# Optimization experiments

Measured on AMD Instinct MI355X. Metric: run time of the kernel, lower is better.

The kernel has to match this reference:

```python
import jax, jax.numpy as jnp
import numpy as np

NUM_HEADS = 32
NUM_KV_HEADS = 8
HEAD_DIM = 128
PAGE_SIZE = 16
NUM_PAGES = 512
PAGES_PER_SEQ = 256  # 4096 cached tokens
Q_LEN = 1024
SCALE = 0.08838834764831845  # 1/sqrt(HEAD_DIM)


def setup_inputs() -> dict:
    key = jax.random.key(0)
    k1, k2, k3, k4, k5 = jax.random.split(key, 5)
    q = jax.random.normal(k1, (Q_LEN, NUM_HEADS * HEAD_DIM), dtype=jnp.float32)
    k = jax.random.normal(k2, (Q_LEN, NUM_KV_HEADS * HEAD_DIM), dtype=jnp.float32)
    v = jax.random.normal(k3, (Q_LEN, NUM_KV_HEADS * HEAD_DIM), dtype=jnp.float32)
    # paged KV cache: [num_pages, 2 (k/v), num_kv_heads, page_size, head_dim]
    kv_cache = jax.random.normal(
        k4, (NUM_PAGES, 2, NUM_KV_HEADS, PAGE_SIZE, HEAD_DIM), dtype=jnp.float32)
    block_table = jnp.sort(
        jax.random.randint(k5, (PAGES_PER_SEQ,), 0, NUM_PAGES, dtype=jnp.int32))
    return {"q": q, "k": k, "v": v, "kv_cache": kv_cache,
            "block_table": block_table}


def reference(q, k, v, kv_cache, block_table):
    # reshape flat projections into heads
    q = q.reshape(-1, NUM_HEADS, HEAD_DIM)          # [Tq, H, D]
    k = k.reshape(-1, NUM_KV_HEADS, HEAD_DIM)       # [Tq, Hkv, D]
    v = v.reshape(-1, NUM_KV_HEADS, HEAD_DIM)

    # gather paged KV cache into continuous tensors (all pages full)
    pages = kv_cache[block_table]                   # [P, 2, Hkv, ps, D]
    # per-page [Hkv, ps, D] -> [ps, Hkv, D], then concat along token dim
    past = jnp.transpose(pages, (1, 0, 3, 2, 4))    # [2, P, ps, Hkv, D]
    past = past.reshape(2, -1, NUM_KV_HEADS, HEAD_DIM)
    past_k, past_v = past[0], past[1]               # [Tpast, Hkv, D]

    k_full = jnp.concatenate([past_k, k], axis=0)   # [Tkv, Hkv, D]
    v_full = jnp.concatenate([past_v, v], axis=0)

    # GQA: repeat kv heads to match query heads
    heads_per_kv = NUM_HEADS // NUM_KV_HEADS
    k_full = jnp.repeat(k_full, heads_per_kv, axis=1)  # [Tkv, H, D]
    v_full = jnp.repeat(v_full, heads_per_kv, axis=1)

    qh = jnp.transpose(q, (1, 0, 2))                # [H, Tq, D]
    kh = jnp.transpose(k_full, (1, 0, 2))           # [H, Tkv, D]
    vh = jnp.transpose(v_full, (1, 0, 2))

    scores = jnp.einsum('hqd,hkd->hqk', qh, kh) * SCALE  # [H, Tq, Tkv]

    # prefill causal mask exactly as in the source: triu(ones(q_len, kv_len), 1)
    q_len, kv_len = qh.shape[1], kh.shape[1]
    causal = jnp.triu(jnp.ones((q_len, kv_len), dtype=bool), k=1)
    scores = jnp.where(causal[None, :, :], -jnp.inf, scores)

    attn = jax.nn.softmax(scores.astype(jnp.float32), axis=-1).astype(qh.dtype)
    out = jnp.einsum('hqk,hkd->hqd', attn, vh)      # [H, Tq, D]
    out = jnp.transpose(out, (1, 0, 2)).reshape(-1, NUM_HEADS * HEAD_DIM)
    return out
```

## Files before the change

kernel.cpp:

```cpp
#include <hip/hip_runtime.h>
#include <hip/hip_bf16.h>


#define Q_STRIDE 4096
#define SCALE 0.08838834764831845f
#define RESCALE_THR 8.0f
#define KSW_TILE 16384
#define VSW_OFF  (2 * 1024 * 1024)
#define ACC1_OFF (4 * 1024 * 1024)
#define ML0_OFF  (ACC1_OFF + 32768 * 256)
#define ML1_OFF  (ML0_OFF + 32768 * 8)

typedef short short8 __attribute__((ext_vector_type(8)));
typedef float f32x4 __attribute__((ext_vector_type(4)));
typedef unsigned short ushort_t;
typedef unsigned int uint_t;

__device__ __forceinline__ ushort_t f2bf(float f) {
    return __builtin_bit_cast(ushort_t, __float2bfloat16(f));
}
__device__ __forceinline__ uint_t pk2(float a, float b) {
    return (uint_t)f2bf(a) | ((uint_t)f2bf(b) << 16);
}
__device__ __forceinline__ float bf2f(ushort_t u) {
    uint_t x = ((uint_t)u) << 16;
    return __builtin_bit_cast(float, x);
}

__launch_bounds__(256)
__global__ void prep_kv(const float* __restrict__ kvc,
                        const int* __restrict__ bt,
                        char* __restrict__ wsb)
{
    __shared__ float sVt[64 * 128];
    const int blk = blockIdx.x;
    const int hkv = blk >> 4;
    const int jb  = blk & 15;
    const int tid = threadIdx.x;
    char* kout = wsb + (size_t)(hkv * 16 + jb) * KSW_TILE;
    char* vout = wsb + VSW_OFF + (size_t)(hkv * 16 + jb) * KSW_TILE;

#pragma unroll
    for (int i = 0; i < 4; ++i) {
        const int u = tid + i * 256;
        const int t = u >> 4, c = u & 15;
        const int gtok = jb * 64 + t;
        const int page = bt[gtok >> 4];
        const float* src = kvc + (size_t)page * 32768 + (size_t)hkv * 2048
                         + (gtok & 15) * 128 + c * 8;
        float4 a = *(const float4*)src;
        float4 b = *(const float4*)(src + 4);
        uint4 p;
        p.x = pk2(a.x, a.y); p.y = pk2(a.z, a.w);
        p.z = pk2(b.x, b.y); p.w = pk2(b.z, b.w);
        *(uint4*)(kout + t * 256 + ((c * 16) ^ ((t & 7) << 4))) = p;
    }
#pragma unroll
    for (int i = 0; i < 8; ++i) {
        const int u = tid + i * 256;
        const int t = u >> 5, c4 = u & 31;
        const int gtok = jb * 64 + t;
        const int page = bt[gtok >> 4];
        const float* src = kvc + (size_t)page * 32768 + 16384
                         + (size_t)hkv * 2048 + (gtok & 15) * 128 + c4 * 4;
        *(float4*)(sVt + t * 128 + c4 * 4) = *(const float4*)src;
    }
    __syncthreads();
#pragma unroll
    for (int i = 0; i < 4; ++i) {
        const int u = tid + i * 256;
        const int d = u >> 3, ch = u & 7;
        float v[8];
#pragma unroll
        for (int k = 0; k < 8; ++k) v[k] = sVt[(8 * ch + k) * 128 + d];
        uint4 p;
        p.x = pk2(v[0], v[1]); p.y = pk2(v[2], v[3]);
        p.z = pk2(v[4], v[5]); p.w = pk2(v[6], v[7]);
        *(uint4*)(vout + ((d * 128 + 16 * ch) ^ ((d & 7) << 4))) = p;
    }
}

#define GLL16(G, L) __builtin_amdgcn_global_load_lds(                         \
    (const uint_t __attribute__((address_space(1)))*)(G),                     \
    (uint_t __attribute__((address_space(3)))*)(L), 16, 0, 0)

#define STAGE(JB, KB, VB) {                                                   \
    const char* b_ = kvbf + (size_t)(hkv * 16 + (JB)) * KSW_TILE              \
                   + w * 1024 + lane * 16;                                    \
    GLL16(b_,                  (KB) + w * 1024);                              \
    GLL16(b_ + 8192,           (KB) + w * 1024 + 8192);                       \
    GLL16(b_ + VSW_OFF,        (VB) + w * 1024);                              \
    GLL16(b_ + VSW_OFF + 8192, (VB) + w * 1024 + 8192);                       \
}

__launch_bounds__(512)
__global__ void attn_main(const float* __restrict__ q,
                          const char* __restrict__ kvbf,
                          float* __restrict__ out,
                          char* __restrict__ wsb)
{
    __shared__ __align__(16) char sK[2][16384];
    __shared__ __align__(16) char sV[2][16384];
    __shared__ __align__(16) char sP[8][2048];

    const int bid  = blockIdx.x;
    const int half = bid >> 8;
    const int rr   = bid & 255;
    const int g    = rr >> 4;
    const int hp   = rr & 15;
    const int qt   = half ? g : (15 - g);
    const int nt   = qt + 1;
    const int nt0  = (nt + 1) >> 1;
    const int jb0  = half ? nt0 : 0;
    const int jb1  = half ? nt  : nt0;
    const int hkv  = hp >> 1;
    const int tid  = threadIdx.x;
    const int w    = tid >> 6;
    const int lane = tid & 63;
    const int l15  = lane & 15;
    const int lhi  = lane >> 4;
    const int h    = hp * 2 + (w >> 2);
    const int rg   = w & 3;

    short8 qf[4];
    {
        const int qrow = qt * 64 + rg * 16 + l15;
        const float* qp = q + (size_t)qrow * Q_STRIDE + h * 128;
#pragma unroll
        for (int s = 0; s < 4; ++s) {
            const int d0 = s * 32 + lhi * 8;
            float4 a = *(const float4*)(qp + d0);
            float4 b = *(const float4*)(qp + d0 + 4);
            short8 v;
            v[0] = (short)f2bf(a.x * SCALE); v[1] = (short)f2bf(a.y * SCALE);
            v[2] = (short)f2bf(a.z * SCALE); v[3] = (short)f2bf(a.w * SCALE);
            v[4] = (short)f2bf(b.x * SCALE); v[5] = (short)f2bf(b.y * SCALE);
            v[6] = (short)f2bf(b.z * SCALE); v[7] = (short)f2bf(b.w * SCALE);
            qf[s] = v;
        }
    }

    f32x4 acc[8];
#pragma unroll
    for (int n2 = 0; n2 < 8; ++n2) acc[n2] = (f32x4){0.f, 0.f, 0.f, 0.f};
    float m_run[4]  = {-1e30f, -1e30f, -1e30f, -1e30f};
    float l_part[4] = {0.f, 0.f, 0.f, 0.f};

    if (jb0 < jb1) {
        STAGE(jb0, sK[0], sV[0])
    }
    __syncthreads();

    for (int jb = jb0; jb < jb1; ++jb) {
        const int cur = (jb - jb0) & 1;
        char* kbuf = sK[cur];
        char* vbuf = sV[cur];
        const bool pf = (jb + 1 < jb1);
        if (pf) {
            STAGE(jb + 1, sK[cur ^ 1], sV[cur ^ 1])
        }

        f32x4 sacc[4];
#pragma unroll
        for (int n = 0; n < 4; ++n) sacc[n] = (f32x4){0.f, 0.f, 0.f, 0.f};
#pragma unroll
        for (int s = 0; s < 4; ++s) {
#pragma unroll
            for (int n = 0; n < 4; ++n) {
                const int tok = n * 16 + l15;
                const uint_t byte = (uint_t)(tok * 256)
                    + (((uint_t)((s * 32 + lhi * 8) * 2)) ^ ((uint_t)((tok & 7) << 4)));
                short8 kb = *(const short8*)(kbuf + byte);
                sacc[n] = __builtin_amdgcn_mfma_f32_16x16x32_bf16(qf[s], kb, sacc[n], 0, 0, 0);
            }
        }

        const bool diag = (jb == qt);
        if (diag) {
#pragma unroll
            for (int n = 0; n < 4; ++n)
#pragma unroll
                for (int j = 0; j < 4; ++j) {
                    const int tok = jb * 64 + n * 16 + l15;
                    const int qg  = qt * 64 + rg * 16 + lhi * 4 + j;
                    if (tok > qg) sacc[n][j] = -1e30f;
                }
        }
#pragma unroll
        for (int j = 0; j < 4; ++j) {
            float lmax = fmaxf(fmaxf(sacc[0][j], sacc[1][j]),
                               fmaxf(sacc[2][j], sacc[3][j]));
            if (__any(lmax > m_run[j] + RESCALE_THR)) {
                float mt = lmax;
#pragma unroll
                for (int off = 1; off < 16; off <<= 1)
                    mt = fmaxf(mt, __shfl_xor(mt, off));
                const float mn = fmaxf(m_run[j], mt);
                const float alpha = __expf(m_run[j] - mn);
                m_run[j] = mn;
                l_part[j] *= alpha;
#pragma unroll
                for (int n2 = 0; n2 < 8; ++n2) acc[n2][j] *= alpha;
            }
            float ls = 0.f;
#pragma unroll
            for (int n = 0; n < 4; ++n) {
                float p = __expf(sacc[n][j] - m_run[j]);
                sacc[n][j] = p;
                ls += p;
            }
            l_part[j] += ls;
        }

        char* pb = sP[w];
#pragma unroll
        for (int n = 0; n < 4; ++n)
#pragma unroll
            for (int j = 0; j < 4; ++j) {
                const int r = lhi * 4 + j;
                const uint_t byte = (uint_t)(r * 128)
                    + (((uint_t)((n * 16 + l15) * 2)) ^ ((uint_t)((r & 7) << 4)));
                *(ushort_t*)(pb + byte) = f2bf(sacc[n][j]);
            }

#pragma unroll
        for (int s2 = 0; s2 < 2; ++s2) {
            const uint_t pbyte = (uint_t)(l15 * 128)
                + (((uint_t)((s2 * 32 + lhi * 8) * 2)) ^ ((uint_t)((l15 & 7) << 4)));
            short8 pa = *(const short8*)(pb + pbyte);
#pragma unroll
            for (int n2 = 0; n2 < 8; ++n2) {
                const int dim = n2 * 16 + l15;
                const uint_t vbyte = (uint_t)(dim * 128)
                    + (((uint_t)((s2 * 32 + lhi * 8) * 2)) ^ ((uint_t)((dim & 7) << 4)));
                short8 vbf = *(const short8*)(vbuf + vbyte);
                acc[n2] = __builtin_amdgcn_mfma_f32_16x16x32_bf16(pa, vbf, acc[n2], 0, 0, 0);
            }
        }

        if (pf) __syncthreads();
    }

#pragma unroll
    for (int j = 0; j < 4; ++j) {
        float lsum = l_part[j];
#pragma unroll
        for (int off = 1; off < 16; off <<= 1)
            lsum += __shfl_xor(lsum, off);
        const int row64 = rg * 16 + lhi * 4 + j;
        const int qg    = qt * 64 + row64;
        const int idx   = (qt * 32 + h) * 64 + row64;
        if (half == 0) {
            float* dst = out + (size_t)qg * Q_STRIDE + h * 128;
#pragma unroll
            for (int n2 = 0; n2 < 8; ++n2)
                dst[n2 * 16 + l15] = acc[n2][j];
            if (l15 == 0) {
                float* ml = (float*)(wsb + ML0_OFF) + (size_t)idx * 2;
                ml[0] = m_run[j]; ml[1] = lsum;
            }
        } else {
            ushort_t* dst = (ushort_t*)(wsb + ACC1_OFF) + (size_t)idx * 128;
#pragma unroll
            for (int n2 = 0; n2 < 8; ++n2)
                dst[n2 * 16 + l15] = f2bf(acc[n2][j]);
            if (l15 == 0) {
                float* ml = (float*)(wsb + ML1_OFF) + (size_t)idx * 2;
                ml[0] = m_run[j]; ml[1] = lsum;
            }
        }
    }
}

__launch_bounds__(256)
__global__ void attn_combine(float* __restrict__ out, const char* __restrict__ wsb)
{
    const int pid = blockIdx.x;
    const int qt = pid >> 5;
    const int h  = pid & 31;
    const int tid = threadIdx.x;
    const int d4  = (tid & 31) * 4;
    const float* ml0b = (const float*)(wsb + ML0_OFF);
    const float* ml1b = (const float*)(wsb + ML1_OFF);
    const ushort_t* a1b = (const ushort_t*)(wsb + ACC1_OFF);

#pragma unroll
    for (int p = 0; p < 8; ++p) {
        const int r = (tid >> 5) + p * 8;
        const size_t idx = (size_t)pid * 64 + r;
        const float m1 = ml0b[idx * 2], l1 = ml0b[idx * 2 + 1];
        const float m2 = ml1b[idx * 2], l2 = ml1b[idx * 2 + 1];
        const float m  = fmaxf(m1, m2);
        const float a1 = __expf(m1 - m), a2 = __expf(m2 - m);
        const float inv = 1.0f / (l1 * a1 + l2 * a2);
        float* o = out + (size_t)(qt * 64 + r) * Q_STRIDE + h * 128 + d4;
        const ushort_t* y4 = a1b + idx * 128 + d4;
        float4 x = *(const float4*)o;
        x.x = (x.x * a1 + bf2f(y4[0]) * a2) * inv;
        x.y = (x.y * a1 + bf2f(y4[1]) * a2) * inv;
        x.z = (x.z * a1 + bf2f(y4[2]) * a2) * inv;
        x.w = (x.w * a1 + bf2f(y4[3]) * a2) * inv;
        *(float4*)o = x;
    }
}

extern "C" void kernel_launch(void* const* d_in, const int* in_sizes, int n_in,
                              void* d_out, int out_size, void* d_ws, size_t ws_size,
                              hipStream_t stream) {
    const float* q   = (const float*)d_in[0];
    const float* kvc = (const float*)d_in[3];
    const int*   bt  = (const int*)d_in[4];
    float* out = (float*)d_out;
    char*  wsb = (char*)d_ws;
    prep_kv<<<dim3(128), dim3(256), 0, stream>>>(kvc, bt, wsb);
    attn_main<<<dim3(512), dim3(512), 0, stream>>>(q, wsb, out, wsb);
    attn_combine<<<dim3(512), dim3(256), 0, stream>>>(out, wsb);
}
```

Baseline: 54.37 us.

## Split attention into per-head 32-token tiles with selective split-KV

```diff
diff --git a/kernel.cpp b/kernel.cpp
--- a/kernel.cpp
+++ b/kernel.cpp
@@ -8,8 +8,8 @@
 #define KSW_TILE 16384
 #define VSW_OFF  (2 * 1024 * 1024)
 #define ACC1_OFF (4 * 1024 * 1024)
-#define ML0_OFF  (ACC1_OFF + 32768 * 256)
-#define ML1_OFF  (ML0_OFF + 32768 * 8)
+#define ML0_OFF  (ACC1_OFF + 16384 * 256)
+#define ML1_OFF  (ML0_OFF + 16384 * 8)
 
 typedef short short8 __attribute__((ext_vector_type(8)));
 typedef float f32x4 __attribute__((ext_vector_type(4)));
@@ -70,13 +70,15 @@
     for (int i = 0; i < 4; ++i) {
         const int u = tid + i * 256;
         const int d = u >> 3, ch = u & 7;
+        const int half = ch >> 2, ch2 = ch & 3;
         float v[8];
 #pragma unroll
-        for (int k = 0; k < 8; ++k) v[k] = sVt[(8 * ch + k) * 128 + d];
+        for (int k = 0; k < 8; ++k)
+            v[k] = sVt[(half * 32 + ch2 * 8 + k) * 128 + d];
         uint4 p;
         p.x = pk2(v[0], v[1]); p.y = pk2(v[2], v[3]);
         p.z = pk2(v[4], v[5]); p.w = pk2(v[6], v[7]);
-        *(uint4*)(vout + ((d * 128 + 16 * ch) ^ ((d & 7) << 4))) = p;
+        *(uint4*)(vout + half * 8192 + d * 64 + ((ch2 * 16) ^ ((d & 3) << 4))) = p;
     }
 }
 
@@ -84,43 +86,50 @@
     (const uint_t __attribute__((address_space(1)))*)(G),                     \
     (uint_t __attribute__((address_space(3)))*)(L), 16, 0, 0)
 
-#define STAGE(JB, KB, VB) {                                                   \
-    const char* b_ = kvbf + (size_t)(hkv * 16 + (JB)) * KSW_TILE              \
-                   + w * 1024 + lane * 16;                                    \
-    GLL16(b_,                  (KB) + w * 1024);                              \
-    GLL16(b_ + 8192,           (KB) + w * 1024 + 8192);                       \
-    GLL16(b_ + VSW_OFF,        (VB) + w * 1024);                              \
-    GLL16(b_ + VSW_OFF + 8192, (VB) + w * 1024 + 8192);                       \
-}
-
-__launch_bounds__(512)
+#define STAGE(JB2, KB, VB) {                                                  \
+    const char* ks_ = kvbf + (size_t)hkv * 262144 + (size_t)(JB2) * 8192      \
+                    + w * 2048 + lane * 16;                                   \
+    GLL16(ks_,                  (KB) + w * 2048);                             \
+    GLL16(ks_ + 1024,           (KB) + w * 2048 + 1024);                      \
+    GLL16(ks_ + VSW_OFF,        (VB) + w * 2048);                             \
+    GLL16(ks_ + VSW_OFF + 1024, (VB) + w * 2048 + 1024);                      \
+}
+
+__launch_bounds__(256)
 __global__ void attn_main(const float* __restrict__ q,
                           const char* __restrict__ kvbf,
                           float* __restrict__ out,
                           char* __restrict__ wsb)
 {
-    __shared__ __align__(16) char sK[2][16384];
-    __shared__ __align__(16) char sV[2][16384];
-    __shared__ __align__(16) char sP[8][2048];
-
-    const int bid  = blockIdx.x;
-    const int half = bid >> 8;
-    const int rr   = bid & 255;
-    const int g    = rr >> 4;
-    const int hp   = rr & 15;
-    const int qt   = half ? g : (15 - g);
-    const int nt   = qt + 1;
-    const int nt0  = (nt + 1) >> 1;
-    const int jb0  = half ? nt0 : 0;
-    const int jb1  = half ? nt  : nt0;
-    const int hkv  = hp >> 1;
+    __shared__ __align__(16) char sK[2][8192];
+    __shared__ __align__(16) char sV[2][8192];
+    __shared__ __align__(16) char sP[4][1024];
+
+    const int bid = blockIdx.x;
+    int qt, jb0, jb1, mode, h;
+    if (bid < 512) {
+        const int half = bid & 1;
+        const int idx  = bid >> 1;
+        qt  = 15 - (idx >> 5);
+        h   = idx & 31;
+        const int nt = qt + 1;
+        jb0 = half ? nt : 0;
+        jb1 = half ? 2 * nt : nt;
+        mode = half ? 2 : 1;
+    } else {
+        const int idx2 = bid - 512;
+        qt  = 7 - (idx2 >> 5);
+        h   = idx2 & 31;
+        jb0 = 0; jb1 = 2 * (qt + 1);
+        mode = 0;
+    }
+    const int hkv = h >> 2;
     const int tid  = threadIdx.x;
     const int w    = tid >> 6;
     const int lane = tid & 63;
     const int l15  = lane & 15;
     const int lhi  = lane >> 4;
-    const int h    = hp * 2 + (w >> 2);
-    const int rg   = w & 3;
+    const int rg   = w;
 
     short8 qf[4];
     {
@@ -146,27 +155,26 @@
     float m_run[4]  = {-1e30f, -1e30f, -1e30f, -1e30f};
     float l_part[4] = {0.f, 0.f, 0.f, 0.f};
 
-    if (jb0 < jb1) {
-        STAGE(jb0, sK[0], sV[0])
-    }
+    STAGE(jb0, sK[0], sV[0])
     __syncthreads();
 
-    for (int jb = jb0; jb < jb1; ++jb) {
-        const int cur = (jb - jb0) & 1;
+    char* pb = sP[w];
+    for (int jb2 = jb0; jb2 < jb1; ++jb2) {
+        const int cur = (jb2 - jb0) & 1;
         char* kbuf = sK[cur];
         char* vbuf = sV[cur];
-        const bool pf = (jb + 1 < jb1);
+        const bool pf = (jb2 + 1 < jb1);
         if (pf) {
-            STAGE(jb + 1, sK[cur ^ 1], sV[cur ^ 1])
-        }
-
-        f32x4 sacc[4];
-#pragma unroll
-        for (int n = 0; n < 4; ++n) sacc[n] = (f32x4){0.f, 0.f, 0.f, 0.f};
+            STAGE(jb2 + 1, sK[cur ^ 1], sV[cur ^ 1])
+        }
+
+        f32x4 sacc[2];
+#pragma unroll
+        for (int n = 0; n < 2; ++n) sacc[n] = (f32x4){0.f, 0.f, 0.f, 0.f};
 #pragma unroll
         for (int s = 0; s < 4; ++s) {
 #pragma unroll
-            for (int n = 0; n < 4; ++n) {
+            for (int n = 0; n < 2; ++n) {
                 const int tok = n * 16 + l15;
                 const uint_t byte = (uint_t)(tok * 256)
                     + (((uint_t)((s * 32 + lhi * 8) * 2)) ^ ((uint_t)((tok & 7) << 4)));
@@ -175,21 +183,19 @@
             }
         }
 
-        const bool diag = (jb == qt);
-        if (diag) {
-#pragma unroll
-            for (int n = 0; n < 4; ++n)
+        if (jb2 >= 2 * qt) {
+#pragma unroll
+            for (int n = 0; n < 2; ++n)
 #pragma unroll
                 for (int j = 0; j < 4; ++j) {
-                    const int tok = jb * 64 + n * 16 + l15;
+                    const int tok = jb2 * 32 + n * 16 + l15;
                     const int qg  = qt * 64 + rg * 16 + lhi * 4 + j;
                     if (tok > qg) sacc[n][j] = -1e30f;
                 }
         }
 #pragma unroll
         for (int j = 0; j < 4; ++j) {
-            float lmax = fmaxf(fmaxf(sacc[0][j], sacc[1][j]),
-                               fmaxf(sacc[2][j], sacc[3][j]));
+            float lmax = fmaxf(sacc[0][j], sacc[1][j]);
             if (__any(lmax > m_run[j] + RESCALE_THR)) {
                 float mt = lmax;
 #pragma unroll
@@ -204,7 +210,7 @@
             }
             float ls = 0.f;
 #pragma unroll
-            for (int n = 0; n < 4; ++n) {
+            for (int n = 0; n < 2; ++n) {
                 float p = __expf(sacc[n][j] - m_run[j]);
                 sacc[n][j] = p;
                 ls += p;
@@ -212,27 +218,25 @@
             l_part[j] += ls;
         }
 
-        char* pb = sP[w];
-#pragma unroll
-        for (int n = 0; n < 4; ++n)
+#pragma unroll
+        for (int n = 0; n < 2; ++n)
 #pragma unroll
             for (int j = 0; j < 4; ++j) {
                 const int r = lhi * 4 + j;
-                const uint_t byte = (uint_t)(r * 128)
-                    + (((uint_t)((n * 16 + l15) * 2)) ^ ((uint_t)((r & 7) << 4)));
+                const uint_t byte = (uint_t)(r * 64)
+                    + (((uint_t)((n * 16 + l15) * 2)) ^ ((uint_t)((r & 3) << 4)));
                 *(ushort_t*)(pb + byte) = f2bf(sacc[n][j]);
             }
 
-#pragma unroll
-        for (int s2 = 0; s2 < 2; ++s2) {
-            const uint_t pbyte = (uint_t)(l15 * 128)
-                + (((uint_t)((s2 * 32 + lhi * 8) * 2)) ^ ((uint_t)((l15 & 7) << 4)));
+        {
+            const uint_t pbyte = (uint_t)(l15 * 64)
+                + (((uint_t)(lhi * 16)) ^ ((uint_t)((l15 & 3) << 4)));
             short8 pa = *(const short8*)(pb + pbyte);
 #pragma unroll
             for (int n2 = 0; n2 < 8; ++n2) {
                 const int dim = n2 * 16 + l15;
-                const uint_t vbyte = (uint_t)(dim * 128)
-                    + (((uint_t)((s2 * 32 + lhi * 8) * 2)) ^ ((uint_t)((dim & 7) << 4)));
+                const uint_t vbyte = (uint_t)(dim * 64)
+                    + (((uint_t)(lhi * 16)) ^ ((uint_t)((dim & 3) << 4)));
                 short8 vbf = *(const short8*)(vbuf + vbyte);
                 acc[n2] = __builtin_amdgcn_mfma_f32_16x16x32_bf16(pa, vbf, acc[n2], 0, 0, 0);
             }
@@ -249,24 +253,32 @@
             lsum += __shfl_xor(lsum, off);
         const int row64 = rg * 16 + lhi * 4 + j;
         const int qg    = qt * 64 + row64;
-        const int idx   = (qt * 32 + h) * 64 + row64;
-        if (half == 0) {
+        if (mode == 0) {
+            const float inv = 1.0f / lsum;
             float* dst = out + (size_t)qg * Q_STRIDE + h * 128;
 #pragma unroll
             for (int n2 = 0; n2 < 8; ++n2)
-                dst[n2 * 16 + l15] = acc[n2][j];
-            if (l15 == 0) {
-                float* ml = (float*)(wsb + ML0_OFF) + (size_t)idx * 2;
-                ml[0] = m_run[j]; ml[1] = lsum;
-            }
+                dst[n2 * 16 + l15] = acc[n2][j] * inv;
         } else {
-            ushort_t* dst = (ushort_t*)(wsb + ACC1_OFF) + (size_t)idx * 128;
-#pragma unroll
-            for (int n2 = 0; n2 < 8; ++n2)
-                dst[n2 * 16 + l15] = f2bf(acc[n2][j]);
-            if (l15 == 0) {
-                float* ml = (float*)(wsb + ML1_OFF) + (size_t)idx * 2;
-                ml[0] = m_run[j]; ml[1] = lsum;
+            const int idx = ((qt - 8) * 32 + h) * 64 + row64;
+            if (mode == 1) {
+                float* dst = out + (size_t)qg * Q_STRIDE + h * 128;
+#pragma unroll
+                for (int n2 = 0; n2 < 8; ++n2)
+                    dst[n2 * 16 + l15] = acc[n2][j];
+                if (l15 == 0) {
+                    float* ml = (float*)(wsb + ML0_OFF) + (size_t)idx * 2;
+                    ml[0] = m_run[j]; ml[1] = lsum;
+                }
+            } else {
+                ushort_t* dst = (ushort_t*)(wsb + ACC1_OFF) + (size_t)idx * 128;
+#pragma unroll
+                for (int n2 = 0; n2 < 8; ++n2)
+                    dst[n2 * 16 + l15] = f2bf(acc[n2][j]);
+                if (l15 == 0) {
+                    float* ml = (float*)(wsb + ML1_OFF) + (size_t)idx * 2;
+                    ml[0] = m_run[j]; ml[1] = lsum;
+                }
             }
         }
     }
@@ -276,7 +288,7 @@
 __global__ void attn_combine(float* __restrict__ out, const char* __restrict__ wsb)
 {
     const int pid = blockIdx.x;
-    const int qt = pid >> 5;
+    const int qt = 8 + (pid >> 5);
     const int h  = pid & 31;
     const int tid = threadIdx.x;
     const int d4  = (tid & 31) * 4;
@@ -313,6 +325,6 @@
     float* out = (float*)d_out;
     char*  wsb = (char*)d_ws;
     prep_kv<<<dim3(128), dim3(256), 0, stream>>>(kvc, bt, wsb);
-    attn_main<<<dim3(512), dim3(512), 0, stream>>>(q, wsb, out, wsb);
-    attn_combine<<<dim3(512), dim3(256), 0, stream>>>(out, wsb);
-}
+    attn_main<<<dim3(768), dim3(256), 0, stream>>>(q, wsb, out, wsb);
+    attn_combine<<<dim3(256), dim3(256), 0, stream>>>(out, wsb);
+}
```

Result: slower. 58.57 us (+7.7%).

## Switch attention to 32x32x16 MFMA with register-resident P and GQA-grouped blocks

Applied to the files above, without the earlier changes.

```diff
diff --git a/kernel.cpp b/kernel.cpp
--- a/kernel.cpp
+++ b/kernel.cpp
@@ -12,9 +12,10 @@
 #define ML1_OFF  (ML0_OFF + 32768 * 8)
 
 typedef short short8 __attribute__((ext_vector_type(8)));
-typedef float f32x4 __attribute__((ext_vector_type(4)));
+typedef float f32x16 __attribute__((ext_vector_type(16)));
+typedef unsigned int uint_t;
+typedef uint_t u32x4 __attribute__((ext_vector_type(4)));
 typedef unsigned short ushort_t;
-typedef unsigned int uint_t;
 
 __device__ __forceinline__ ushort_t f2bf(float f) {
     return __builtin_bit_cast(ushort_t, __float2bfloat16(f));
@@ -53,7 +54,7 @@
         uint4 p;
         p.x = pk2(a.x, a.y); p.y = pk2(a.z, a.w);
         p.z = pk2(b.x, b.y); p.w = pk2(b.z, b.w);
-        *(uint4*)(kout + t * 256 + ((c * 16) ^ ((t & 7) << 4))) = p;
+        *(uint4*)(kout + t * 256 + ((c ^ (t & 15)) << 4)) = p;
     }
 #pragma unroll
     for (int i = 0; i < 8; ++i) {
@@ -76,7 +77,7 @@
         uint4 p;
         p.x = pk2(v[0], v[1]); p.y = pk2(v[2], v[3]);
         p.z = pk2(v[4], v[5]); p.w = pk2(v[6], v[7]);
-        *(uint4*)(vout + ((d * 128 + 16 * ch) ^ ((d & 7) << 4))) = p;
+        *(uint4*)(vout + d * 128 + ((ch ^ (d & 7)) << 4)) = p;
     }
 }
 
@@ -86,14 +87,18 @@
 
 #define STAGE(JB, KB, VB) {                                                   \
     const char* b_ = kvbf + (size_t)(hkv * 16 + (JB)) * KSW_TILE              \
-                   + w * 1024 + lane * 16;                                    \
-    GLL16(b_,                  (KB) + w * 1024);                              \
-    GLL16(b_ + 8192,           (KB) + w * 1024 + 8192);                       \
-    GLL16(b_ + VSW_OFF,        (VB) + w * 1024);                              \
-    GLL16(b_ + VSW_OFF + 8192, (VB) + w * 1024 + 8192);                       \
-}
-
-__launch_bounds__(512)
+                   + w * 4096 + lane * 16;                                    \
+    GLL16(b_,                  (KB) + w * 4096);                              \
+    GLL16(b_ + 1024,           (KB) + w * 4096 + 1024);                       \
+    GLL16(b_ + 2048,           (KB) + w * 4096 + 2048);                       \
+    GLL16(b_ + 3072,           (KB) + w * 4096 + 3072);                       \
+    GLL16(b_ + VSW_OFF,        (VB) + w * 4096);                              \
+    GLL16(b_ + VSW_OFF + 1024, (VB) + w * 4096 + 1024);                       \
+    GLL16(b_ + VSW_OFF + 2048, (VB) + w * 4096 + 2048);                       \
+    GLL16(b_ + VSW_OFF + 3072, (VB) + w * 4096 + 3072);                       \
+}
+
+__launch_bounds__(256)
 __global__ void attn_main(const float* __restrict__ q,
                           const char* __restrict__ kvbf,
                           float* __restrict__ out,
@@ -101,34 +106,30 @@
 {
     __shared__ __align__(16) char sK[2][16384];
     __shared__ __align__(16) char sV[2][16384];
-    __shared__ __align__(16) char sP[8][2048];
 
     const int bid  = blockIdx.x;
     const int half = bid >> 8;
-    const int rr   = bid & 255;
-    const int g    = rr >> 4;
-    const int hp   = rr & 15;
-    const int qt   = half ? g : (15 - g);
-    const int nt   = qt + 1;
+    const int r8   = bid & 255;
+    const int hkv  = r8 >> 5;
+    const int rt   = r8 & 31;
+    const int nt   = (rt >> 1) + 1;
     const int nt0  = (nt + 1) >> 1;
     const int jb0  = half ? nt0 : 0;
-    const int jb1  = half ? nt  : nt0;
-    const int hkv  = hp >> 1;
+    const int jb1  = half ? nt : nt0;
     const int tid  = threadIdx.x;
     const int w    = tid >> 6;
     const int lane = tid & 63;
-    const int l15  = lane & 15;
-    const int lhi  = lane >> 4;
-    const int h    = hp * 2 + (w >> 2);
-    const int rg   = w & 3;
-
-    short8 qf[4];
+    const int l31  = lane & 31;
+    const int hi   = lane >> 5;
+    const int hi4  = hi * 4;
+    const int h    = hkv * 4 + w;
+
+    short8 qf[8];
     {
-        const int qrow = qt * 64 + rg * 16 + l15;
-        const float* qp = q + (size_t)qrow * Q_STRIDE + h * 128;
-#pragma unroll
-        for (int s = 0; s < 4; ++s) {
-            const int d0 = s * 32 + lhi * 8;
+        const float* qp = q + (size_t)(rt * 32 + l31) * Q_STRIDE + h * 128;
+#pragma unroll
+        for (int ks = 0; ks < 8; ++ks) {
+            const int d0 = ks * 16 + hi * 8;
             float4 a = *(const float4*)(qp + d0);
             float4 b = *(const float4*)(qp + d0 + 4);
             short8 v;
@@ -136,15 +137,17 @@
             v[2] = (short)f2bf(a.z * SCALE); v[3] = (short)f2bf(a.w * SCALE);
             v[4] = (short)f2bf(b.x * SCALE); v[5] = (short)f2bf(b.y * SCALE);
             v[6] = (short)f2bf(b.z * SCALE); v[7] = (short)f2bf(b.w * SCALE);
-            qf[s] = v;
-        }
-    }
-
-    f32x4 acc[8];
-#pragma unroll
-    for (int n2 = 0; n2 < 8; ++n2) acc[n2] = (f32x4){0.f, 0.f, 0.f, 0.f};
-    float m_run[4]  = {-1e30f, -1e30f, -1e30f, -1e30f};
-    float l_part[4] = {0.f, 0.f, 0.f, 0.f};
+            qf[ks] = v;
+        }
+    }
+
+    f32x16 acc[4];
+#pragma unroll
+    for (int db = 0; db < 4; ++db)
+#pragma unroll
+        for (int r = 0; r < 16; ++r) acc[db][r] = 0.f;
+    float m_run  = -1e30f;
+    float l_part = 0.f;
 
     if (jb0 < jb1) {
         STAGE(jb0, sK[0], sV[0])
@@ -153,121 +156,135 @@
 
     for (int jb = jb0; jb < jb1; ++jb) {
         const int cur = (jb - jb0) & 1;
-        char* kbuf = sK[cur];
-        char* vbuf = sV[cur];
+        const char* kbuf = sK[cur];
+        const char* vbuf = sV[cur];
         const bool pf = (jb + 1 < jb1);
         if (pf) {
             STAGE(jb + 1, sK[cur ^ 1], sV[cur ^ 1])
         }
 
-        f32x4 sacc[4];
-#pragma unroll
-        for (int n = 0; n < 4; ++n) sacc[n] = (f32x4){0.f, 0.f, 0.f, 0.f};
-#pragma unroll
-        for (int s = 0; s < 4; ++s) {
-#pragma unroll
-            for (int n = 0; n < 4; ++n) {
-                const int tok = n * 16 + l15;
-                const uint_t byte = (uint_t)(tok * 256)
-                    + (((uint_t)((s * 32 + lhi * 8) * 2)) ^ ((uint_t)((tok & 7) << 4)));
-                short8 kb = *(const short8*)(kbuf + byte);
-                sacc[n] = __builtin_amdgcn_mfma_f32_16x16x32_bf16(qf[s], kb, sacc[n], 0, 0, 0);
-            }
-        }
-
-        const bool diag = (jb == qt);
+        f32x16 s0, s1;
+#pragma unroll
+        for (int r = 0; r < 16; ++r) { s0[r] = 0.f; s1[r] = 0.f; }
+        __builtin_amdgcn_s_setprio(1);
+#pragma unroll
+        for (int ks = 0; ks < 8; ++ks) {
+            const uint_t c0 = (uint_t)(((ks * 2 + hi) ^ (l31 & 15)) << 4);
+            short8 ka0 = *(const short8*)(kbuf + l31 * 256 + c0);
+            short8 ka1 = *(const short8*)(kbuf + 8192 + l31 * 256 + c0);
+            s0 = __builtin_amdgcn_mfma_f32_32x32x16_bf16(ka0, qf[ks], s0, 0, 0, 0);
+            s1 = __builtin_amdgcn_mfma_f32_32x32x16_bf16(ka1, qf[ks], s1, 0, 0, 0);
+        }
+        __builtin_amdgcn_s_setprio(0);
+
+        const bool diag = (jb == nt - 1);
         if (diag) {
-#pragma unroll
-            for (int n = 0; n < 4; ++n)
-#pragma unroll
-                for (int j = 0; j < 4; ++j) {
-                    const int tok = jb * 64 + n * 16 + l15;
-                    const int qg  = qt * 64 + rg * 16 + lhi * 4 + j;
-                    if (tok > qg) sacc[n][j] = -1e30f;
+            if (rt & 1) {
+#pragma unroll
+                for (int r = 0; r < 16; ++r) {
+                    const int treg = (r & 3) + 8 * (r >> 2) + hi4;
+                    if (treg > l31) s1[r] = -1e30f;
                 }
-        }
-#pragma unroll
-        for (int j = 0; j < 4; ++j) {
-            float lmax = fmaxf(fmaxf(sacc[0][j], sacc[1][j]),
-                               fmaxf(sacc[2][j], sacc[3][j]));
-            if (__any(lmax > m_run[j] + RESCALE_THR)) {
-                float mt = lmax;
-#pragma unroll
-                for (int off = 1; off < 16; off <<= 1)
-                    mt = fmaxf(mt, __shfl_xor(mt, off));
-                const float mn = fmaxf(m_run[j], mt);
-                const float alpha = __expf(m_run[j] - mn);
-                m_run[j] = mn;
-                l_part[j] *= alpha;
-#pragma unroll
-                for (int n2 = 0; n2 < 8; ++n2) acc[n2][j] *= alpha;
-            }
-            float ls = 0.f;
-#pragma unroll
-            for (int n = 0; n < 4; ++n) {
-                float p = __expf(sacc[n][j] - m_run[j]);
-                sacc[n][j] = p;
-                ls += p;
-            }
-            l_part[j] += ls;
-        }
-
-        char* pb = sP[w];
-#pragma unroll
-        for (int n = 0; n < 4; ++n)
-#pragma unroll
-            for (int j = 0; j < 4; ++j) {
-                const int r = lhi * 4 + j;
-                const uint_t byte = (uint_t)(r * 128)
-                    + (((uint_t)((n * 16 + l15) * 2)) ^ ((uint_t)((r & 7) << 4)));
-                *(ushort_t*)(pb + byte) = f2bf(sacc[n][j]);
-            }
-
-#pragma unroll
-        for (int s2 = 0; s2 < 2; ++s2) {
-            const uint_t pbyte = (uint_t)(l15 * 128)
-                + (((uint_t)((s2 * 32 + lhi * 8) * 2)) ^ ((uint_t)((l15 & 7) << 4)));
-            short8 pa = *(const short8*)(pb + pbyte);
-#pragma unroll
-            for (int n2 = 0; n2 < 8; ++n2) {
-                const int dim = n2 * 16 + l15;
-                const uint_t vbyte = (uint_t)(dim * 128)
-                    + (((uint_t)((s2 * 32 + lhi * 8) * 2)) ^ ((uint_t)((dim & 7) << 4)));
-                short8 vbf = *(const short8*)(vbuf + vbyte);
-                acc[n2] = __builtin_amdgcn_mfma_f32_16x16x32_bf16(pa, vbf, acc[n2], 0, 0, 0);
-            }
-        }
+            } else {
+#pragma unroll
+                for (int r = 0; r < 16; ++r) {
+                    const int treg = (r & 3) + 8 * (r >> 2) + hi4;
+                    if (treg > l31) s0[r] = -1e30f;
+                    s1[r] = -1e30f;
+                }
+            }
+        }
+
+        float pm = s0[0];
+#pragma unroll
+        for (int r = 1; r < 16; ++r) pm = fmaxf(pm, s0[r]);
+#pragma unroll
+        for (int r = 0; r < 16; ++r) pm = fmaxf(pm, s1[r]);
+        const float rmax = fmaxf(pm, __shfl_xor(pm, 32));
+        if (__any(rmax > m_run + RESCALE_THR)) {
+            const float mn = fmaxf(m_run, rmax);
+            const float al = __expf(m_run - mn);
+            m_run = mn;
+            l_part *= al;
+#pragma unroll
+            for (int r = 0; r < 16; ++r) {
+                const float ar = __shfl(al, (r & 3) + 8 * (r >> 2) + hi4);
+#pragma unroll
+                for (int db = 0; db < 4; ++db) acc[db][r] *= ar;
+            }
+        }
+        float ls = 0.f;
+#pragma unroll
+        for (int r = 0; r < 16; ++r) {
+            float e0 = __expf(s0[r] - m_run);
+            float e1 = __expf(s1[r] - m_run);
+            s0[r] = e0; s1[r] = e1;
+            ls += e0 + e1;
+        }
+        l_part += ls;
+
+        short8 pa[4];
+#pragma unroll
+        for (int hf = 0; hf < 2; ++hf) {
+            const f32x16& s = hf ? s1 : s0;
+            uint_t w0 = pk2(s[0],  s[1]),  w1 = pk2(s[2],  s[3]);
+            uint_t w2 = pk2(s[4],  s[5]),  w3 = pk2(s[6],  s[7]);
+            uint_t w4 = pk2(s[8],  s[9]),  w5 = pk2(s[10], s[11]);
+            uint_t w6 = pk2(s[12], s[13]), w7 = pk2(s[14], s[15]);
+            const uint_t sA = __shfl_xor(hi ? w0 : w2, 32);
+            const uint_t sB = __shfl_xor(hi ? w1 : w3, 32);
+            const uint_t sC = __shfl_xor(hi ? w4 : w6, 32);
+            const uint_t sD = __shfl_xor(hi ? w5 : w7, 32);
+            u32x4 f0, f1;
+            f0[0] = hi ? sA : w0; f0[1] = hi ? sB : w1;
+            f0[2] = hi ? w2 : sA; f0[3] = hi ? w3 : sB;
+            f1[0] = hi ? sC : w4; f1[1] = hi ? sD : w5;
+            f1[2] = hi ? w6 : sC; f1[3] = hi ? w7 : sD;
+            pa[hf * 2]     = __builtin_bit_cast(short8, f0);
+            pa[hf * 2 + 1] = __builtin_bit_cast(short8, f1);
+        }
+
+        __builtin_amdgcn_s_setprio(1);
+#pragma unroll
+        for (int kf = 0; kf < 4; ++kf) {
+#pragma unroll
+            for (int db = 0; db < 4; ++db) {
+                const uint_t byte = (uint_t)(db * 4096 + l31 * 128)
+                    + (uint_t)((((kf << 1) + hi) ^ (l31 & 7)) << 4);
+                short8 vb = *(const short8*)(vbuf + byte);
+                acc[db] = __builtin_amdgcn_mfma_f32_32x32x16_bf16(pa[kf], vb, acc[db], 0, 0, 0);
+            }
+        }
+        __builtin_amdgcn_s_setprio(0);
 
         if (pf) __syncthreads();
     }
 
-#pragma unroll
-    for (int j = 0; j < 4; ++j) {
-        float lsum = l_part[j];
-#pragma unroll
-        for (int off = 1; off < 16; off <<= 1)
-            lsum += __shfl_xor(lsum, off);
-        const int row64 = rg * 16 + lhi * 4 + j;
-        const int qg    = qt * 64 + row64;
-        const int idx   = (qt * 32 + h) * 64 + row64;
-        if (half == 0) {
-            float* dst = out + (size_t)qg * Q_STRIDE + h * 128;
-#pragma unroll
-            for (int n2 = 0; n2 < 8; ++n2)
-                dst[n2 * 16 + l15] = acc[n2][j];
-            if (l15 == 0) {
-                float* ml = (float*)(wsb + ML0_OFF) + (size_t)idx * 2;
-                ml[0] = m_run[j]; ml[1] = lsum;
-            }
-        } else {
-            ushort_t* dst = (ushort_t*)(wsb + ACC1_OFF) + (size_t)idx * 128;
-#pragma unroll
-            for (int n2 = 0; n2 < 8; ++n2)
-                dst[n2 * 16 + l15] = f2bf(acc[n2][j]);
-            if (l15 == 0) {
-                float* ml = (float*)(wsb + ML1_OFF) + (size_t)idx * 2;
-                ml[0] = m_run[j]; ml[1] = lsum;
-            }
+    const float l_row = l_part + __shfl_xor(l_part, 32);
+    if (half == 0) {
+#pragma unroll
+        for (int db = 0; db < 4; ++db)
+#pragma unroll
+            for (int r = 0; r < 16; ++r) {
+                const int qg = rt * 32 + (r & 3) + 8 * (r >> 2) + hi4;
+                out[(size_t)qg * Q_STRIDE + h * 128 + db * 32 + l31] = acc[db][r];
+            }
+        if (lane < 32) {
+            float* ml = (float*)(wsb + ML0_OFF) + (size_t)(h * 1024 + rt * 32 + l31) * 2;
+            ml[0] = m_run; ml[1] = l_row;
+        }
+    } else {
+        ushort_t* a1b = (ushort_t*)(wsb + ACC1_OFF);
+#pragma unroll
+        for (int db = 0; db < 4; ++db)
+#pragma unroll
+            for (int r = 0; r < 16; ++r) {
+                const int qg = rt * 32 + (r & 3) + 8 * (r >> 2) + hi4;
+                a1b[(size_t)(h * 1024 + qg) * 128 + db * 32 + l31] = f2bf(acc[db][r]);
+            }
+        if (lane < 32) {
+            float* ml = (float*)(wsb + ML1_OFF) + (size_t)(h * 1024 + rt * 32 + l31) * 2;
+            ml[0] = m_run; ml[1] = l_row;
         }
     }
 }
@@ -276,8 +293,8 @@
 __global__ void attn_combine(float* __restrict__ out, const char* __restrict__ wsb)
 {
     const int pid = blockIdx.x;
-    const int qt = pid >> 5;
-    const int h  = pid & 31;
+    const int h   = pid >> 4;
+    const int qb  = (pid & 15) * 64;
     const int tid = threadIdx.x;
     const int d4  = (tid & 31) * 4;
     const float* ml0b = (const float*)(wsb + ML0_OFF);
@@ -287,13 +304,13 @@
 #pragma unroll
     for (int p = 0; p < 8; ++p) {
         const int r = (tid >> 5) + p * 8;
-        const size_t idx = (size_t)pid * 64 + r;
+        const size_t idx = (size_t)h * 1024 + qb + r;
         const float m1 = ml0b[idx * 2], l1 = ml0b[idx * 2 + 1];
         const float m2 = ml1b[idx * 2], l2 = ml1b[idx * 2 + 1];
         const float m  = fmaxf(m1, m2);
         const float a1 = __expf(m1 - m), a2 = __expf(m2 - m);
         const float inv = 1.0f / (l1 * a1 + l2 * a2);
-        float* o = out + (size_t)(qt * 64 + r) * Q_STRIDE + h * 128 + d4;
+        float* o = out + (size_t)(qb + r) * Q_STRIDE + h * 128 + d4;
         const ushort_t* y4 = a1b + idx * 128 + d4;
         float4 x = *(const float4*)o;
         x.x = (x.x * a1 + bf2f(y4[0]) * a2) * inv;
@@ -313,6 +330,6 @@
     float* out = (float*)d_out;
     char*  wsb = (char*)d_ws;
     prep_kv<<<dim3(128), dim3(256), 0, stream>>>(kvc, bt, wsb);
-    attn_main<<<dim3(512), dim3(512), 0, stream>>>(q, wsb, out, wsb);
+    attn_main<<<dim3(512), dim3(256), 0, stream>>>(q, wsb, out, wsb);
     attn_combine<<<dim3(512), dim3(256), 0, stream>>>(out, wsb);
 }
```

Result: slower. 61.20 us (+12.6%).

## Restructure attention work split: two heads per wave, split only long q-tiles

Applied to the files above, without the earlier changes.

```diff
diff --git a/kernel.cpp b/kernel.cpp
--- a/kernel.cpp
+++ b/kernel.cpp
@@ -8,8 +8,8 @@
 #define KSW_TILE 16384
 #define VSW_OFF  (2 * 1024 * 1024)
 #define ACC1_OFF (4 * 1024 * 1024)
-#define ML0_OFF  (ACC1_OFF + 32768 * 256)
-#define ML1_OFF  (ML0_OFF + 32768 * 8)
+#define ML0_OFF  (ACC1_OFF + 16384 * 256)
+#define ML1_OFF  (ML0_OFF + 16384 * 8)
 
 typedef short short8 __attribute__((ext_vector_type(8)));
 typedef float f32x4 __attribute__((ext_vector_type(4)));
@@ -85,15 +85,64 @@
     (uint_t __attribute__((address_space(3)))*)(L), 16, 0, 0)
 
 #define STAGE(JB, KB, VB) {                                                   \
-    const char* b_ = kvbf + (size_t)(hkv * 16 + (JB)) * KSW_TILE              \
-                   + w * 1024 + lane * 16;                                    \
-    GLL16(b_,                  (KB) + w * 1024);                              \
-    GLL16(b_ + 8192,           (KB) + w * 1024 + 8192);                       \
-    GLL16(b_ + VSW_OFF,        (VB) + w * 1024);                              \
-    GLL16(b_ + VSW_OFF + 8192, (VB) + w * 1024 + 8192);                       \
-}
-
-__launch_bounds__(512)
+    const char* ks = kvbf + (size_t)(hkv * 16 + (JB)) * KSW_TILE              \
+                   + w * 4096 + lane * 16;                                    \
+    const char* vs = ks + VSW_OFF;                                            \
+    _Pragma("unroll")                                                         \
+    for (int i = 0; i < 4; ++i) {                                             \
+        GLL16(ks + i * 1024, (KB) + w * 4096 + i * 1024);                     \
+        GLL16(vs + i * 1024, (VB) + w * 4096 + i * 1024);                     \
+    }                                                                         \
+}
+
+#define SOFTMAX_P(SACC, MRUN, LPART, ACC, PB) {                               \
+    if (diag) {                                                               \
+        _Pragma("unroll")                                                     \
+        for (int n = 0; n < 4; ++n)                                           \
+            _Pragma("unroll")                                                 \
+            for (int j = 0; j < 4; ++j) {                                     \
+                const int tok = jb * 64 + n * 16 + l15;                       \
+                const int qg  = qt * 64 + rg * 16 + lhi * 4 + j;              \
+                if (tok > qg) SACC[n][j] = -1e30f;                            \
+            }                                                                 \
+    }                                                                         \
+    _Pragma("unroll")                                                         \
+    for (int j = 0; j < 4; ++j) {                                             \
+        float lmax = fmaxf(fmaxf(SACC[0][j], SACC[1][j]),                     \
+                           fmaxf(SACC[2][j], SACC[3][j]));                    \
+        if (__any(lmax > MRUN[j] + RESCALE_THR)) {                            \
+            float mt = lmax;                                                  \
+            _Pragma("unroll")                                                 \
+            for (int off = 1; off < 16; off <<= 1)                            \
+                mt = fmaxf(mt, __shfl_xor(mt, off));                          \
+            const float mn = fmaxf(MRUN[j], mt);                              \
+            const float alpha = __expf(MRUN[j] - mn);                         \
+            MRUN[j] = mn;                                                     \
+            LPART[j] *= alpha;                                                \
+            _Pragma("unroll")                                                 \
+            for (int n2 = 0; n2 < 8; ++n2) ACC[n2][j] *= alpha;               \
+        }                                                                     \
+        float ls = 0.f;                                                       \
+        _Pragma("unroll")                                                     \
+        for (int n = 0; n < 4; ++n) {                                         \
+            float p = __expf(SACC[n][j] - MRUN[j]);                           \
+            SACC[n][j] = p;                                                   \
+            ls += p;                                                          \
+        }                                                                     \
+        LPART[j] += ls;                                                       \
+    }                                                                         \
+    _Pragma("unroll")                                                         \
+    for (int n = 0; n < 4; ++n)                                               \
+        _Pragma("unroll")                                                     \
+        for (int j = 0; j < 4; ++j) {                                         \
+            const int r = lhi * 4 + j;                                        \
+            const uint_t byte = (uint_t)(r * 128)                             \
+                + (((uint_t)((n * 16 + l15) * 2)) ^ ((uint_t)((r & 7) << 4)));\
+            *(ushort_t*)((PB) + byte) = f2bf(SACC[n][j]);                     \
+        }                                                                     \
+}
+
+__launch_bounds__(256)
 __global__ void attn_main(const float* __restrict__ q,
                           const char* __restrict__ kvbf,
                           float* __restrict__ out,
@@ -101,31 +150,44 @@
 {
     __shared__ __align__(16) char sK[2][16384];
     __shared__ __align__(16) char sV[2][16384];
-    __shared__ __align__(16) char sP[8][2048];
-
-    const int bid  = blockIdx.x;
-    const int half = bid >> 8;
-    const int rr   = bid & 255;
-    const int g    = rr >> 4;
-    const int hp   = rr & 15;
-    const int qt   = half ? g : (15 - g);
-    const int nt   = qt + 1;
-    const int nt0  = (nt + 1) >> 1;
-    const int jb0  = half ? nt0 : 0;
-    const int jb1  = half ? nt  : nt0;
-    const int hkv  = hp >> 1;
+    __shared__ __align__(16) char sP[4][2][2048];
+
+    const int bid = blockIdx.x;
+    int qt, jb0, jb1, h0, hkv, mode;
+    bool two;
+    if (bid < 256) {
+        const int half = bid & 1;
+        const int idx  = bid >> 1;
+        qt  = 15 - (idx >> 4);
+        const int hp = idx & 15;
+        h0  = hp * 2;
+        hkv = hp >> 1;
+        const int nt  = qt + 1;
+        const int nt0 = (nt + 1) >> 1;
+        jb0 = half ? nt0 : 0;
+        jb1 = half ? nt : nt0;
+        mode = half ? 2 : 1;
+        two = true;
+    } else {
+        const int didx = bid - 256;
+        qt  = 7 - (didx >> 5);
+        h0  = didx & 31;
+        hkv = h0 >> 2;
+        jb0 = 0; jb1 = qt + 1;
+        mode = 0;
+        two = false;
+    }
     const int tid  = threadIdx.x;
     const int w    = tid >> 6;
     const int lane = tid & 63;
     const int l15  = lane & 15;
     const int lhi  = lane >> 4;
-    const int h    = hp * 2 + (w >> 2);
-    const int rg   = w & 3;
-
-    short8 qf[4];
+    const int rg   = w;
+
+    short8 qfA[4], qfB[4];
     {
         const int qrow = qt * 64 + rg * 16 + l15;
-        const float* qp = q + (size_t)qrow * Q_STRIDE + h * 128;
+        const float* qp = q + (size_t)qrow * Q_STRIDE + h0 * 128;
 #pragma unroll
         for (int s = 0; s < 4; ++s) {
             const int d0 = s * 32 + lhi * 8;
@@ -136,19 +198,32 @@
             v[2] = (short)f2bf(a.z * SCALE); v[3] = (short)f2bf(a.w * SCALE);
             v[4] = (short)f2bf(b.x * SCALE); v[5] = (short)f2bf(b.y * SCALE);
             v[6] = (short)f2bf(b.z * SCALE); v[7] = (short)f2bf(b.w * SCALE);
-            qf[s] = v;
-        }
-    }
-
-    f32x4 acc[8];
-#pragma unroll
-    for (int n2 = 0; n2 < 8; ++n2) acc[n2] = (f32x4){0.f, 0.f, 0.f, 0.f};
-    float m_run[4]  = {-1e30f, -1e30f, -1e30f, -1e30f};
-    float l_part[4] = {0.f, 0.f, 0.f, 0.f};
-
-    if (jb0 < jb1) {
-        STAGE(jb0, sK[0], sV[0])
-    }
+            qfA[s] = v;
+            if (two) {
+                float4 a2 = *(const float4*)(qp + 128 + d0);
+                float4 b2 = *(const float4*)(qp + 128 + d0 + 4);
+                short8 v2;
+                v2[0] = (short)f2bf(a2.x * SCALE); v2[1] = (short)f2bf(a2.y * SCALE);
+                v2[2] = (short)f2bf(a2.z * SCALE); v2[3] = (short)f2bf(a2.w * SCALE);
+                v2[4] = (short)f2bf(b2.x * SCALE); v2[5] = (short)f2bf(b2.y * SCALE);
+                v2[6] = (short)f2bf(b2.z * SCALE); v2[7] = (short)f2bf(b2.w * SCALE);
+                qfB[s] = v2;
+            }
+        }
+    }
+
+    f32x4 accA[8], accB[8];
+#pragma unroll
+    for (int n2 = 0; n2 < 8; ++n2) {
+        accA[n2] = (f32x4){0.f, 0.f, 0.f, 0.f};
+        accB[n2] = (f32x4){0.f, 0.f, 0.f, 0.f};
+    }
+    float mA[4] = {-1e30f, -1e30f, -1e30f, -1e30f};
+    float lA[4] = {0.f, 0.f, 0.f, 0.f};
+    float mB[4] = {-1e30f, -1e30f, -1e30f, -1e30f};
+    float lB[4] = {0.f, 0.f, 0.f, 0.f};
+
+    STAGE(jb0, sK[0], sV[0])
     __syncthreads();
 
     for (int jb = jb0; jb < jb1; ++jb) {
@@ -158,11 +233,20 @@
         const bool pf = (jb + 1 < jb1);
         if (pf) {
             STAGE(jb + 1, sK[cur ^ 1], sV[cur ^ 1])
-        }
-
-        f32x4 sacc[4];
-#pragma unroll
-        for (int n = 0; n < 4; ++n) sacc[n] = (f32x4){0.f, 0.f, 0.f, 0.f};
+            asm volatile("s_waitcnt vmcnt(8)" ::: "memory");
+        } else {
+            asm volatile("s_waitcnt vmcnt(0)" ::: "memory");
+        }
+        __builtin_amdgcn_sched_barrier(0);
+        __builtin_amdgcn_s_barrier();
+        __builtin_amdgcn_sched_barrier(0);
+
+        f32x4 saccA[4], saccB[4];
+#pragma unroll
+        for (int n = 0; n < 4; ++n) {
+            saccA[n] = (f32x4){0.f, 0.f, 0.f, 0.f};
+            saccB[n] = (f32x4){0.f, 0.f, 0.f, 0.f};
+        }
 #pragma unroll
         for (int s = 0; s < 4; ++s) {
 #pragma unroll
@@ -171,102 +255,89 @@
                 const uint_t byte = (uint_t)(tok * 256)
                     + (((uint_t)((s * 32 + lhi * 8) * 2)) ^ ((uint_t)((tok & 7) << 4)));
                 short8 kb = *(const short8*)(kbuf + byte);
-                sacc[n] = __builtin_amdgcn_mfma_f32_16x16x32_bf16(qf[s], kb, sacc[n], 0, 0, 0);
+                saccA[n] = __builtin_amdgcn_mfma_f32_16x16x32_bf16(qfA[s], kb, saccA[n], 0, 0, 0);
+                if (two)
+                    saccB[n] = __builtin_amdgcn_mfma_f32_16x16x32_bf16(qfB[s], kb, saccB[n], 0, 0, 0);
             }
         }
 
         const bool diag = (jb == qt);
-        if (diag) {
-#pragma unroll
-            for (int n = 0; n < 4; ++n)
-#pragma unroll
-                for (int j = 0; j < 4; ++j) {
-                    const int tok = jb * 64 + n * 16 + l15;
-                    const int qg  = qt * 64 + rg * 16 + lhi * 4 + j;
-                    if (tok > qg) sacc[n][j] = -1e30f;
-                }
-        }
-#pragma unroll
-        for (int j = 0; j < 4; ++j) {
-            float lmax = fmaxf(fmaxf(sacc[0][j], sacc[1][j]),
-                               fmaxf(sacc[2][j], sacc[3][j]));
-            if (__any(lmax > m_run[j] + RESCALE_THR)) {
-                float mt = lmax;
-#pragma unroll
-                for (int off = 1; off < 16; off <<= 1)
-                    mt = fmaxf(mt, __shfl_xor(mt, off));
-                const float mn = fmaxf(m_run[j], mt);
-                const float alpha = __expf(m_run[j] - mn);
-                m_run[j] = mn;
-                l_part[j] *= alpha;
-#pragma unroll
-                for (int n2 = 0; n2 < 8; ++n2) acc[n2][j] *= alpha;
-            }
-            float ls = 0.f;
-#pragma unroll
-            for (int n = 0; n < 4; ++n) {
-                float p = __expf(sacc[n][j] - m_run[j]);
-                sacc[n][j] = p;
-                ls += p;
-            }
-            l_part[j] += ls;
-        }
-
-        char* pb = sP[w];
-#pragma unroll
-        for (int n = 0; n < 4; ++n)
-#pragma unroll
-            for (int j = 0; j < 4; ++j) {
-                const int r = lhi * 4 + j;
-                const uint_t byte = (uint_t)(r * 128)
-                    + (((uint_t)((n * 16 + l15) * 2)) ^ ((uint_t)((r & 7) << 4)));
-                *(ushort_t*)(pb + byte) = f2bf(sacc[n][j]);
-            }
+        SOFTMAX_P(saccA, mA, lA, accA, sP[w][0])
+        if (two) {
+            SOFTMAX_P(saccB, mB, lB, accB, sP[w][1])
+        }
 
 #pragma unroll
         for (int s2 = 0; s2 < 2; ++s2) {
             const uint_t pbyte = (uint_t)(l15 * 128)
                 + (((uint_t)((s2 * 32 + lhi * 8) * 2)) ^ ((uint_t)((l15 & 7) << 4)));
-            short8 pa = *(const short8*)(pb + pbyte);
+            short8 paA = *(const short8*)(sP[w][0] + pbyte);
+            short8 paB = *(const short8*)(sP[w][1] + pbyte);
 #pragma unroll
             for (int n2 = 0; n2 < 8; ++n2) {
                 const int dim = n2 * 16 + l15;
                 const uint_t vbyte = (uint_t)(dim * 128)
                     + (((uint_t)((s2 * 32 + lhi * 8) * 2)) ^ ((uint_t)((dim & 7) << 4)));
                 short8 vbf = *(const short8*)(vbuf + vbyte);
-                acc[n2] = __builtin_amdgcn_mfma_f32_16x16x32_bf16(pa, vbf, acc[n2], 0, 0, 0);
-            }
-        }
-
-        if (pf) __syncthreads();
+                accA[n2] = __builtin_amdgcn_mfma_f32_16x16x32_bf16(paA, vbf, accA[n2], 0, 0, 0);
+                if (two)
+                    accB[n2] = __builtin_amdgcn_mfma_f32_16x16x32_bf16(paB, vbf, accB[n2], 0, 0, 0);
+            }
+        }
+
+        if (pf) {
+            __builtin_amdgcn_sched_barrier(0);
+            __builtin_amdgcn_s_barrier();
+        }
     }
 
 #pragma unroll
     for (int j = 0; j < 4; ++j) {
-        float lsum = l_part[j];
-#pragma unroll
-        for (int off = 1; off < 16; off <<= 1)
-            lsum += __shfl_xor(lsum, off);
+        float lsA = lA[j];
+        float lsB = lB[j];
+#pragma unroll
+        for (int off = 1; off < 16; off <<= 1) {
+            lsA += __shfl_xor(lsA, off);
+            lsB += __shfl_xor(lsB, off);
+        }
         const int row64 = rg * 16 + lhi * 4 + j;
         const int qg    = qt * 64 + row64;
-        const int idx   = (qt * 32 + h) * 64 + row64;
-        if (half == 0) {
-            float* dst = out + (size_t)qg * Q_STRIDE + h * 128;
+        if (mode == 0) {
+            const float inv = 1.0f / lsA;
+            float* dst = out + (size_t)qg * Q_STRIDE + h0 * 128;
 #pragma unroll
             for (int n2 = 0; n2 < 8; ++n2)
-                dst[n2 * 16 + l15] = acc[n2][j];
+                dst[n2 * 16 + l15] = accA[n2][j] * inv;
+        } else if (mode == 1) {
+            float* dA = out + (size_t)qg * Q_STRIDE + h0 * 128;
+            float* dB = dA + 128;
+#pragma unroll
+            for (int n2 = 0; n2 < 8; ++n2) {
+                dA[n2 * 16 + l15] = accA[n2][j];
+                dB[n2 * 16 + l15] = accB[n2][j];
+            }
             if (l15 == 0) {
-                float* ml = (float*)(wsb + ML0_OFF) + (size_t)idx * 2;
-                ml[0] = m_run[j]; ml[1] = lsum;
+                const int ia = h0 * 512 + (qt - 8) * 64 + row64;
+                float* ml = (float*)(wsb + ML0_OFF);
+                ml[(size_t)ia * 2]           = mA[j];
+                ml[(size_t)ia * 2 + 1]       = lsA;
+                ml[(size_t)(ia + 512) * 2]     = mB[j];
+                ml[(size_t)(ia + 512) * 2 + 1] = lsB;
             }
         } else {
-            ushort_t* dst = (ushort_t*)(wsb + ACC1_OFF) + (size_t)idx * 128;
-#pragma unroll
-            for (int n2 = 0; n2 < 8; ++n2)
-                dst[n2 * 16 + l15] = f2bf(acc[n2][j]);
+            ushort_t* ab = (ushort_t*)(wsb + ACC1_OFF);
+            const int ia = h0 * 512 + (qt - 8) * 64 + row64;
+#pragma unroll
+            for (int n2 = 0; n2 < 8; ++n2) {
+                ab[(size_t)ia * 128 + n2 * 16 + l15]         = f2bf(accA[n2][j]);
+                ab[(size_t)(ia + 512) * 128 + n2 * 16 + l15] = f2bf(accB[n2][j]);
+            }
             if (l15 == 0) {
-                float* ml = (float*)(wsb + ML1_OFF) + (size_t)idx * 2;
-                ml[0] = m_run[j]; ml[1] = lsum;
+                float* ml = (float*)(wsb + ML1_OFF);
+                ml[(size_t)ia * 2]           = mA[j];
+                ml[(size_t)ia * 2 + 1]       = lsA;
+                ml[(size_t)(ia + 512) * 2]     = mB[j];
+                ml[(size_t)(ia + 512) * 2 + 1] = lsB;
             }
         }
     }
@@ -276,7 +347,7 @@
 __global__ void attn_combine(float* __restrict__ out, const char* __restrict__ wsb)
 {
     const int pid = blockIdx.x;
-    const int qt = pid >> 5;
+    const int qt = 8 + (pid >> 5);
     const int h  = pid & 31;
     const int tid = threadIdx.x;
     const int d4  = (tid & 31) * 4;
@@ -287,7 +358,7 @@
 #pragma unroll
     for (int p = 0; p < 8; ++p) {
         const int r = (tid >> 5) + p * 8;
-        const size_t idx = (size_t)pid * 64 + r;
+        const size_t idx = (size_t)h * 512 + (qt - 8) * 64 + r;
         const float m1 = ml0b[idx * 2], l1 = ml0b[idx * 2 + 1];
         const float m2 = ml1b[idx * 2], l2 = ml1b[idx * 2 + 1];
         const float m  = fmaxf(m1, m2);
@@ -313,6 +384,6 @@
     float* out = (float*)d_out;
     char*  wsb = (char*)d_ws;
     prep_kv<<<dim3(128), dim3(256), 0, stream>>>(kvc, bt, wsb);
-    attn_main<<<dim3(512), dim3(512), 0, stream>>>(q, wsb, out, wsb);
-    attn_combine<<<dim3(512), dim3(256), 0, stream>>>(out, wsb);
-}
+    attn_main<<<dim3(512), dim3(256), 0, stream>>>(q, wsb, out, wsb);
+    attn_combine<<<dim3(256), dim3(256), 0, stream>>>(out, wsb);
+}
```

After: 90.28 us. +66.0%, slower.
